# Kernel tuning notes

Measured on AMD Instinct MI355X. Metric: run time of the kernel, lower is better.

Reference implementation:

```python
import jax, jax.numpy as jnp
import numpy as np

B, S, D, H = 2, 2048, 768, 12
DK = D // H  # 64
LN_EPS = 1e-5


def setup_inputs() -> dict:
    key = jax.random.key(0)
    ks = jax.random.split(key, 8)
    std = 0.02
    return {
        "x": jax.random.normal(ks[0], (B, S, D), dtype=jnp.float32),
        "Wq": jax.random.normal(ks[1], (D, D), dtype=jnp.float32) * std,
        "Wp": jax.random.normal(ks[2], (D, D), dtype=jnp.float32) * std,
        "Wk": jax.random.normal(ks[3], (D, D), dtype=jnp.float32) * std,
        "Wv": jax.random.normal(ks[4], (D, D), dtype=jnp.float32) * std,
        "Wo": jax.random.normal(ks[5], (D, D), dtype=jnp.float32) * std,
        "bo": jnp.zeros((D,), dtype=jnp.float32),
        "gamma": jnp.ones((D,), dtype=jnp.float32),
        "beta": jnp.zeros((D,), dtype=jnp.float32),
        "dt": jnp.asarray(0.1, dtype=jnp.float32),
        "gate": jnp.ones((1,), dtype=jnp.float32),
    }


def _heads(t):
    # [B,S,D] -> [B,H,S,DK]
    return t.reshape(B, S, H, DK).transpose(0, 2, 1, 3)


def reference(x, Wq, Wp, Wk, Wv, Wo, bo, gamma, beta, dt, gate):
    scale = DK ** -0.5
    q = _heads(x @ Wq)
    p = _heads(x @ Wp)
    k = _heads(x @ Wk)
    v = _heads(x @ Wv)

    # --- first attention pass (potential energy at q) ---
    e1 = jnp.einsum("bhsd,bhtd->bhst", q, k) * scale
    w1 = jax.nn.softmax(e1, axis=-1)
    pe1 = jnp.einsum("bhst,bhtd->bhsd", w1, v)  # dV/dq approx (v_to_k = Identity since d_v == d_k)

    # --- leapfrog half step + full position step ---
    p_half = p - (dt / 2) * pe1 * gate
    q_new = q + dt * p_half

    # --- second attention pass at updated q ---
    e2 = jnp.einsum("bhsd,bhtd->bhst", q_new, k) * scale
    w2 = jax.nn.softmax(e2, axis=-1)
    pe2 = jnp.einsum("bhst,bhtd->bhsd", w2, v)
    p_new = p_half - (dt / 2) * pe2 * gate

    q_flat = q_new.transpose(0, 2, 1, 3).reshape(B, S, D)
    out = q_flat @ Wo + bo + x  # to_output + residual

    mu = jnp.mean(out, axis=-1, keepdims=True)
    var = jnp.mean(jnp.square(out - mu), axis=-1, keepdims=True)
    return (out - mu) * jax.lax.rsqrt(var + LN_EPS) * gamma + beta
```

## Files before the change

### kernel.cpp

```cpp
#include <hip/hip_runtime.h>
#include <stdint.h>

typedef __bf16 bf16;
typedef __bf16 bf16x8 __attribute__((ext_vector_type(8)));
typedef __bf16 bf16x4 __attribute__((ext_vector_type(4)));
typedef float f32x4 __attribute__((ext_vector_type(4)));

constexpr int nB = 2, nS = 2048, nD = 768, nH = 12, nDK = 64;
constexpr int nM = nB * nS;
constexpr float LN_EPS = 1e-5f;

static __device__ __forceinline__ f32x4 mfma16(bf16x8 a, bf16x8 b, f32x4 c) {
  return __builtin_amdgcn_mfma_f32_16x16x32_bf16(a, b, c, 0, 0, 0);
}

static __device__ __forceinline__ void gll16(const void* g, void* l) {
  __builtin_amdgcn_global_load_lds(
      (const __attribute__((address_space(1))) void*)g,
      (__attribute__((address_space(3))) void*)l, 16, 0, 0);
}

__global__ __launch_bounds__(256) void k_prep_x(const float* __restrict__ x,
                                                bf16* __restrict__ xb) {
  int i = (blockIdx.x * 256 + threadIdx.x) * 4;
  float4 v = *(const float4*)(x + i);
  bf16x4 o;
  o[0] = (bf16)v.x; o[1] = (bf16)v.y; o[2] = (bf16)v.z; o[3] = (bf16)v.w;
  *(bf16x4*)(xb + i) = o;
}

__global__ __launch_bounds__(256) void k_prep_w(
    const float* __restrict__ w0, const float* __restrict__ w1,
    const float* __restrict__ w2, const float* __restrict__ w3,
    const float* __restrict__ w4, bf16* __restrict__ wt) {
  __shared__ float tb[64][65];
  int w = blockIdx.z;
  const float* src = (w == 0) ? w0 : (w == 1) ? w1 : (w == 2) ? w2 : (w == 3) ? w3 : w4;
  int k0 = blockIdx.y * 64, n0 = blockIdx.x * 64;
  int tx = threadIdx.x & 63, ty = threadIdx.x >> 6;
#pragma unroll
  for (int it = 0; it < 16; ++it) {
    int r = it * 4 + ty;
    tb[r][tx] = src[(size_t)(k0 + r) * nD + n0 + tx];
  }
  __syncthreads();
  bf16* dst = wt + (size_t)w * nD * nD;
#pragma unroll
  for (int it = 0; it < 16; ++it) {
    int r = it * 4 + ty;
    dst[(size_t)(n0 + r) * nD + k0 + tx] = (bf16)tb[tx][r];
  }
}

__global__ __launch_bounds__(256, 2) void k_gemm_qpkv(
    const bf16* __restrict__ xb, const bf16* __restrict__ wt,
    bf16* __restrict__ qf, bf16* __restrict__ pf, bf16* __restrict__ kf_,
    bf16* __restrict__ vt) {
  __shared__ alignas(16) char smem[65536];
  int t = threadIdx.x, lane = t & 63, w = t >> 6;
  int fr = lane & 15, fg = lane >> 4;
  int wm = w >> 1, wn = w & 1;
  int widx = blockIdx.z;
  int m0 = blockIdx.y * 128, n0 = blockIdx.x * 128;
  const bf16* abase = xb + (size_t)m0 * nD;
  const bf16* bbase = wt + (size_t)widx * nD * nD + (size_t)n0 * nD;

  f32x4 acc[4][4];
#pragma unroll
  for (int i = 0; i < 4; ++i)
#pragma unroll
    for (int j = 0; j < 4; ++j) acc[i][j] = (f32x4){0.f, 0.f, 0.f, 0.f};

  int aoff[2][4], boff[2][4];
#pragma unroll
  for (int ks = 0; ks < 2; ++ks) {
#pragma unroll
    for (int i = 0; i < 4; ++i) {
      int row = wm * 64 + i * 16 + fr;
      aoff[ks][i] = row * 128 + (((ks * 4 + fg) ^ (row & 7)) << 4);
      int rowb = wn * 64 + i * 16 + fr;
      boff[ks][i] = 16384 + rowb * 128 + (((ks * 4 + fg) ^ (rowb & 7)) << 4);
    }
  }
  const bf16 *asrc[4], *bsrc[4];
#pragma unroll
  for (int i = 0; i < 4; ++i) {
    int row = i * 32 + (t >> 3);
    int c = (t & 7) ^ (row & 7);
    asrc[i] = abase + (size_t)row * nD + c * 8;
    bsrc[i] = bbase + (size_t)row * nD + c * 8;
  }

#define STAGEG(BUF, kt)                                                        \
  {                                                                            \
    _Pragma("unroll") for (int i = 0; i < 4; ++i) {                            \
      gll16(asrc[i] + (kt)*64, smem + (BUF) + i * 4096 + w * 1024);            \
      gll16(bsrc[i] + (kt)*64, smem + (BUF) + 16384 + i * 4096 + w * 1024);    \
    }                                                                          \
  }

#define COMPUTEG(BUF)                                                          \
  {                                                                            \
    _Pragma("unroll") for (int ks = 0; ks < 2; ++ks) {                         \
      bf16x8 af[4], bfr[4];                                                    \
      _Pragma("unroll") for (int i = 0; i < 4; ++i)                            \
          af[i] = *(const bf16x8*)(smem + (BUF) + aoff[ks][i]);                \
      _Pragma("unroll") for (int j = 0; j < 4; ++j)                            \
          bfr[j] = *(const bf16x8*)(smem + (BUF) + boff[ks][j]);               \
      _Pragma("unroll") for (int i = 0; i < 4; ++i)                            \
          _Pragma("unroll") for (int j = 0; j < 4; ++j) acc[i][j] =            \
          mfma16(af[i], bfr[j], acc[i][j]);                                    \
    }                                                                          \
  }

  STAGEG(0, 0);
  __syncthreads();
#pragma unroll 1
  for (int kt = 0; kt < 12; kt += 2) {
    if (kt + 1 < 12) STAGEG(32768, kt + 1);
    COMPUTEG(0);
    __syncthreads();
    if (kt + 2 < 12) STAGEG(0, kt + 2);
    COMPUTEG(32768);
    __syncthreads();
  }
#undef STAGEG
#undef COMPUTEG

  if (widx < 3) {
    bf16* outf = (widx == 0) ? qf : (widx == 1) ? pf : kf_;
    float oscale = (widx == 2) ? 0.18033688f : 1.0f;
#pragma unroll
    for (int i = 0; i < 4; ++i)
#pragma unroll
      for (int j = 0; j < 4; ++j) {
        int n = n0 + wn * 64 + j * 16 + fr;
#pragma unroll
        for (int r = 0; r < 4; ++r) {
          int m = m0 + wm * 64 + i * 16 + fg * 4 + r;
          outf[(size_t)m * nD + n] = (bf16)(acc[i][j][r] * oscale);
        }
      }
  } else {
#pragma unroll
    for (int i = 0; i < 4; ++i)
#pragma unroll
      for (int j = 0; j < 4; ++j) {
        int n = n0 + wn * 64 + j * 16 + fr;
        int h = n >> 6, dk = n & 63;
        int mbase = m0 + wm * 64 + i * 16 + fg * 4;
        int b = mbase >> 11, s = mbase & (nS - 1);
        int bh = b * nH + h;
        bf16x4 pk;
#pragma unroll
        for (int r = 0; r < 4; ++r) pk[r] = (bf16)acc[i][j][r];
        *(bf16x4*)(vt + ((size_t)bh * nDK + dk) * nS + s) = pk;
      }
  }
}

__global__ __launch_bounds__(256, 3) void k_attn(
    const bf16* __restrict__ qf, const bf16* __restrict__ pf,
    const bf16* __restrict__ kf_, const bf16* __restrict__ vt,
    const float* __restrict__ dtp, const float* __restrict__ gatep,
    bf16* __restrict__ qn) {
  __shared__ alignas(16) char lds[40960];
  int t = threadIdx.x, lane = t & 63, w = t >> 6;
  int fr = lane & 15, fg = lane >> 4;
  int blk = blockIdx.x;
  int qt = blk & 31, bh = blk >> 5;
  int b = bh / nH, h = bh % nH;
  int q0 = qt * 64 + w * 16;
  const bf16* Qrow = qf + (size_t)(b * nS) * nD + (size_t)h * nDK;
  const bf16* Prow = pf + (size_t)(b * nS) * nD + (size_t)h * nDK;
  const bf16* Krow = kf_ + (size_t)(b * nS) * nD + (size_t)h * nDK;
  const bf16* Vb = vt + (size_t)bh * nDK * nS;
  char* myp = lds + 32768 + w * 2048;

  bf16x8 qa[2];
#pragma unroll
  for (int ks = 0; ks < 2; ++ks)
    qa[ks] = *(const bf16x8*)(Qrow + (size_t)(q0 + fr) * nD + ks * 32 + fg * 8);

  bf16x8 vone;
#pragma unroll
  for (int i = 0; i < 8; ++i) vone[i] = (bf16)1.0f;

  f32x4 o[5];
#pragma unroll
  for (int df = 0; df < 5; ++df) o[df] = (f32x4){0.f, 0.f, 0.f, 0.f};

  int koA[4], koB[4];
#pragma unroll
  for (int kfi = 0; kfi < 4; ++kfi) {
    int key = kfi * 16 + fr;
    koA[kfi] = key * 128 + ((fg ^ (key & 7)) << 4);
    koB[kfi] = key * 128 + (((4 + fg) ^ (key & 7)) << 4);
  }
  int vo[2][4], pr[2], pw[4];
#pragma unroll
  for (int ks = 0; ks < 2; ++ks) {
    pr[ks] = fr * 128 + (((ks * 4 + fg) ^ (fr & 7)) << 4);
#pragma unroll
    for (int df = 0; df < 4; ++df) {
      int row = df * 16 + fr;
      vo[ks][df] = row * 128 + (((ks * 4 + fg) ^ (row & 7)) << 4);
    }
  }
#pragma unroll
  for (int kfi = 0; kfi < 4; ++kfi) {
    int blk16 = kfi * 2 + (fg >> 1);
    pw[kfi] = fr * 128 + (((blk16 ^ (fr & 7)) << 4) | ((fg & 1) << 3));
  }

  const bf16 *ks0, *ks1, *vs0, *vs1;
  {
    int r0 = w * 16 + (lane >> 3), c0 = (lane & 7) ^ (r0 & 7);
    int r1 = r0 + 8, c1 = (lane & 7) ^ (r1 & 7);
    ks0 = Krow + (size_t)r0 * nD + c0 * 8;
    ks1 = Krow + (size_t)r1 * nD + c1 * 8;
    vs0 = Vb + (size_t)r0 * nS + c0 * 8;
    vs1 = Vb + (size_t)r1 * nS + c1 * 8;
  }

#define STAGE(KB, VB, kt)                                                      \
  {                                                                            \
    gll16(ks0 + (size_t)(kt)*64 * nD, lds + (KB) + w * 2048);                  \
    gll16(vs0 + (kt)*64, lds + (VB) + w * 2048);                               \
    gll16(ks1 + (size_t)(kt)*64 * nD, lds + (KB) + w * 2048 + 1024);           \
    gll16(vs1 + (kt)*64, lds + (VB) + w * 2048 + 1024);                        \
  }

#define COMPUTE(KB, VB)                                                        \
  {                                                                            \
    f32x4 sf[4];                                                               \
    _Pragma("unroll") for (int kfi = 0; kfi < 4; ++kfi) {                      \
      bf16x8 ka = *(const bf16x8*)(lds + (KB) + koA[kfi]);                     \
      bf16x8 kc = *(const bf16x8*)(lds + (KB) + koB[kfi]);                     \
      f32x4 s = mfma16(ka, qa[0], (f32x4){0.f, 0.f, 0.f, 0.f});                \
      sf[kfi] = mfma16(kc, qa[1], s);                                          \
    }                                                                          \
    _Pragma("unroll") for (int kfi = 0; kfi < 4; ++kfi) {                      \
      bf16x4 pk;                                                               \
      _Pragma("unroll") for (int r = 0; r < 4; ++r)                            \
          pk[r] = (bf16)__builtin_exp2f(sf[kfi][r]);                           \
      *(bf16x4*)(myp + pw[kfi]) = pk;                                          \
    }                                                                          \
    _Pragma("unroll") for (int ks = 0; ks < 2; ++ks) {                         \
      bf16x8 pb = *(const bf16x8*)(myp + pr[ks]);                              \
      _Pragma("unroll") for (int df = 0; df < 4; ++df) {                       \
        bf16x8 vv = *(const bf16x8*)(lds + (VB) + vo[ks][df]);                 \
        o[df] = mfma16(vv, pb, o[df]);                                         \
      }                                                                        \
      o[4] = mfma16(vone, pb, o[4]);                                           \
    }                                                                          \
  }

#define VMCNT4 asm volatile("s_waitcnt vmcnt(4)" ::: "memory")
#define VMCNT0 asm volatile("s_waitcnt vmcnt(0)" ::: "memory")
#define BAR __builtin_amdgcn_s_barrier()

  STAGE(0, 16384, 0);
#pragma unroll 1
  for (int kt = 0; kt < 32; kt += 2) {
    STAGE(8192, 24576, kt + 1);
    VMCNT4;
    BAR;
    COMPUTE(0, 16384);
    BAR;
    if (kt + 2 < 32) {
      STAGE(0, 16384, kt + 2);
      VMCNT4;
    } else {
      VMCNT0;
    }
    BAR;
    COMPUTE(8192, 24576);
    BAR;
  }
#undef STAGE
#undef COMPUTE
#undef VMCNT4
#undef VMCNT0
#undef BAR

  float dt = dtp[0], gate = gatep[0];
  float c2 = 0.5f * dt * dt * gate;
  float inv = 1.f / o[4][0];
  int qrow = q0 + fr;
#pragma unroll
  for (int df = 0; df < 4; ++df) {
    int dk = df * 16 + fg * 4;
    bf16x4 qv4 = *(const bf16x4*)(Qrow + (size_t)qrow * nD + dk);
    bf16x4 pv4 = *(const bf16x4*)(Prow + (size_t)qrow * nD + dk);
    bf16x4 ov;
#pragma unroll
    for (int r = 0; r < 4; ++r) {
      float pe = o[df][r] * inv;
      ov[r] = (bf16)((float)qv4[r] + dt * (float)pv4[r] - c2 * pe);
    }
    *(bf16x4*)(qn + ((size_t)(b * nS) + qrow) * nD + h * nDK + dk) = ov;
  }
}

__global__ __launch_bounds__(256, 2) void k_gemm_out(
    const bf16* __restrict__ qn, const bf16* __restrict__ wto,
    const float* __restrict__ bo, const float* __restrict__ x,
    float* __restrict__ outp) {
  __shared__ alignas(16) char smem[65536];
  int t = threadIdx.x, lane = t & 63, w = t >> 6;
  int fr = lane & 15, fg = lane >> 4;
  int wm = w >> 1, wn = w & 1;
  int m0 = blockIdx.y * 128, n0 = blockIdx.x * 128;
  const bf16* abase = qn + (size_t)m0 * nD;
  const bf16* bbase = wto + (size_t)n0 * nD;

  f32x4 acc[4][4];
#pragma unroll
  for (int i = 0; i < 4; ++i)
#pragma unroll
    for (int j = 0; j < 4; ++j) acc[i][j] = (f32x4){0.f, 0.f, 0.f, 0.f};

  int aoff[2][4], boff[2][4];
#pragma unroll
  for (int ks = 0; ks < 2; ++ks) {
#pragma unroll
    for (int i = 0; i < 4; ++i) {
      int row = wm * 64 + i * 16 + fr;
      aoff[ks][i] = row * 128 + (((ks * 4 + fg) ^ (row & 7)) << 4);
      int rowb = wn * 64 + i * 16 + fr;
      boff[ks][i] = 16384 + rowb * 128 + (((ks * 4 + fg) ^ (rowb & 7)) << 4);
    }
  }
  const bf16 *asrc[4], *bsrc[4];
#pragma unroll
  for (int i = 0; i < 4; ++i) {
    int row = i * 32 + (t >> 3);
    int c = (t & 7) ^ (row & 7);
    asrc[i] = abase + (size_t)row * nD + c * 8;
    bsrc[i] = bbase + (size_t)row * nD + c * 8;
  }

#define STAGEG(BUF, kt)                                                        \
  {                                                                            \
    _Pragma("unroll") for (int i = 0; i < 4; ++i) {                            \
      gll16(asrc[i] + (kt)*64, smem + (BUF) + i * 4096 + w * 1024);            \
      gll16(bsrc[i] + (kt)*64, smem + (BUF) + 16384 + i * 4096 + w * 1024);    \
    }                                                                          \
  }

#define COMPUTEG(BUF)                                                          \
  {                                                                            \
    _Pragma("unroll") for (int ks = 0; ks < 2; ++ks) {                         \
      bf16x8 af[4], bfr[4];                                                    \
      _Pragma("unroll") for (int i = 0; i < 4; ++i)                            \
          af[i] = *(const bf16x8*)(smem + (BUF) + aoff[ks][i]);                \
      _Pragma("unroll") for (int j = 0; j < 4; ++j)                            \
          bfr[j] = *(const bf16x8*)(smem + (BUF) + boff[ks][j]);               \
      _Pragma("unroll") for (int i = 0; i < 4; ++i)                            \
          _Pragma("unroll") for (int j = 0; j < 4; ++j) acc[i][j] =            \
          mfma16(af[i], bfr[j], acc[i][j]);                                    \
    }                                                                          \
  }

  STAGEG(0, 0);
  __syncthreads();
#pragma unroll 1
  for (int kt = 0; kt < 12; kt += 2) {
    if (kt + 1 < 12) STAGEG(32768, kt + 1);
    COMPUTEG(0);
    __syncthreads();
    if (kt + 2 < 12) STAGEG(0, kt + 2);
    COMPUTEG(32768);
    __syncthreads();
  }
#undef STAGEG
#undef COMPUTEG

#pragma unroll
  for (int i = 0; i < 4; ++i)
#pragma unroll
    for (int j = 0; j < 4; ++j) {
      int n = n0 + wn * 64 + j * 16 + fr;
      float bias = bo[n];
#pragma unroll
      for (int r = 0; r < 4; ++r) {
        int m = m0 + wm * 64 + i * 16 + fg * 4 + r;
        outp[(size_t)m * nD + n] = acc[i][j][r] + bias + x[(size_t)m * nD + n];
      }
    }
}

__global__ __launch_bounds__(256) void k_ln(const float* outp,
                                            const float* __restrict__ gamma,
                                            const float* __restrict__ beta,
                                            float* y) {
  int t = threadIdx.x, lane = t & 63, w = t >> 6;
  int row = blockIdx.x * 4 + w;
  const float* rp = outp + (size_t)row * nD;
  float v[12], s1 = 0.f, s2 = 0.f;
#pragma unroll
  for (int i = 0; i < 12; ++i) {
    v[i] = rp[lane + i * 64];
    s1 += v[i];
    s2 += v[i] * v[i];
  }
#pragma unroll
  for (int d = 1; d < 64; d <<= 1) {
    s1 += __shfl_xor(s1, d);
    s2 += __shfl_xor(s2, d);
  }
  float mu = s1 * (1.f / 768.f);
  float var = s2 * (1.f / 768.f) - mu * mu;
  float rstd = rsqrtf(var + LN_EPS);
  float* yp = y + (size_t)row * nD;
#pragma unroll
  for (int i = 0; i < 12; ++i) {
    int n = lane + i * 64;
    yp[n] = (v[i] - mu) * rstd * gamma[n] + beta[n];
  }
}

extern "C" void kernel_launch(void* const* d_in, const int* in_sizes, int n_in,
                              void* d_out, int out_size, void* d_ws, size_t ws_size,
                              hipStream_t stream) {
  const float* x = (const float*)d_in[0];
  const float* Wq = (const float*)d_in[1];
  const float* Wp = (const float*)d_in[2];
  const float* Wk = (const float*)d_in[3];
  const float* Wv = (const float*)d_in[4];
  const float* Wo = (const float*)d_in[5];
  const float* bo = (const float*)d_in[6];
  const float* gamma = (const float*)d_in[7];
  const float* beta = (const float*)d_in[8];
  const float* dt = (const float*)d_in[9];
  const float* gate = (const float*)d_in[10];

  char* ws = (char*)d_ws;
  const size_t szb = (size_t)nM * nD * 2;
  bf16* xb = (bf16*)(ws + 0 * szb);
  bf16* qf = (bf16*)(ws + 1 * szb);
  bf16* pf = (bf16*)(ws + 2 * szb);
  bf16* kf_ = (bf16*)(ws + 3 * szb);
  bf16* vt = (bf16*)(ws + 4 * szb);
  bf16* wt = (bf16*)(ws + 5 * szb);
  bf16* qn = xb;
  float* outp = (float*)d_out;

  k_prep_x<<<dim3(nM * nD / 1024), dim3(256), 0, stream>>>(x, xb);
  k_prep_w<<<dim3(12, 12, 5), dim3(256), 0, stream>>>(Wq, Wp, Wk, Wv, Wo, wt);
  k_gemm_qpkv<<<dim3(6, 32, 4), dim3(256), 0, stream>>>(xb, wt, qf, pf, kf_, vt);
  k_attn<<<dim3(768), dim3(256), 0, stream>>>(qf, pf, kf_, vt, dt, gate, qn);
  k_gemm_out<<<dim3(6, 32), dim3(256), 0, stream>>>(qn, wt + 4 * (size_t)nD * nD, bo, x, outp);
  k_ln<<<dim3(nM / 4), dim3(256), 0, stream>>>(outp, gamma, beta, (float*)d_out);
}
```

Baseline: 115.3 us.

## Process two query row-groups per wave in attention to reuse K/V fragments

The attention kernel now runs 128 threads (2 waves) per block, and each wave handles 32 query rows instead of 16. Each K and V fragment read from LDS is reused for two query groups, which halves LDS reads per MFMA. Each wave also issues twice as many global-to-LDS loads per stage, with the wait count adjusted to match. The trade-off is more registers per wave and fewer waves per block to hide latency, which may lower occupancy.

```diff
diff --git a/kernel.cpp b/kernel.cpp
--- a/kernel.cpp
+++ b/kernel.cpp
@@ -159,7 +159,7 @@
   }
 }
 
-__global__ __launch_bounds__(256, 3) void k_attn(
+__global__ __launch_bounds__(128, 2) void k_attn(
     const bf16* __restrict__ qf, const bf16* __restrict__ pf,
     const bf16* __restrict__ kf_, const bf16* __restrict__ vt,
     const float* __restrict__ dtp, const float* __restrict__ gatep,
@@ -170,25 +170,30 @@
   int blk = blockIdx.x;
   int qt = blk & 31, bh = blk >> 5;
   int b = bh / nH, h = bh % nH;
-  int q0 = qt * 64 + w * 16;
+  int q0 = qt * 64 + w * 32;
   const bf16* Qrow = qf + (size_t)(b * nS) * nD + (size_t)h * nDK;
   const bf16* Prow = pf + (size_t)(b * nS) * nD + (size_t)h * nDK;
   const bf16* Krow = kf_ + (size_t)(b * nS) * nD + (size_t)h * nDK;
   const bf16* Vb = vt + (size_t)bh * nDK * nS;
-  char* myp = lds + 32768 + w * 2048;
-
-  bf16x8 qa[2];
-#pragma unroll
-  for (int ks = 0; ks < 2; ++ks)
-    qa[ks] = *(const bf16x8*)(Qrow + (size_t)(q0 + fr) * nD + ks * 32 + fg * 8);
+  char* myp = lds + 32768 + w * 4096;
+
+  bf16x8 qa[2][2];
+#pragma unroll
+  for (int qg = 0; qg < 2; ++qg)
+#pragma unroll
+    for (int ks = 0; ks < 2; ++ks)
+      qa[qg][ks] = *(const bf16x8*)(Qrow + (size_t)(q0 + qg * 16 + fr) * nD +
+                                    ks * 32 + fg * 8);
 
   bf16x8 vone;
 #pragma unroll
   for (int i = 0; i < 8; ++i) vone[i] = (bf16)1.0f;
 
-  f32x4 o[5];
-#pragma unroll
-  for (int df = 0; df < 5; ++df) o[df] = (f32x4){0.f, 0.f, 0.f, 0.f};
+  f32x4 o[2][5];
+#pragma unroll
+  for (int qg = 0; qg < 2; ++qg)
+#pragma unroll
+    for (int df = 0; df < 5; ++df) o[qg][df] = (f32x4){0.f, 0.f, 0.f, 0.f};
 
   int koA[4], koB[4];
 #pragma unroll
@@ -213,50 +218,57 @@
     pw[kfi] = fr * 128 + (((blk16 ^ (fr & 7)) << 4) | ((fg & 1) << 3));
   }
 
-  const bf16 *ks0, *ks1, *vs0, *vs1;
+  const bf16 *ksrc[4], *vsrc[4];
   {
-    int r0 = w * 16 + (lane >> 3), c0 = (lane & 7) ^ (r0 & 7);
-    int r1 = r0 + 8, c1 = (lane & 7) ^ (r1 & 7);
-    ks0 = Krow + (size_t)r0 * nD + c0 * 8;
-    ks1 = Krow + (size_t)r1 * nD + c1 * 8;
-    vs0 = Vb + (size_t)r0 * nS + c0 * 8;
-    vs1 = Vb + (size_t)r1 * nS + c1 * 8;
+    int c = (lane & 7) ^ (lane >> 3);
+#pragma unroll
+    for (int i = 0; i < 4; ++i) {
+      int row = w * 32 + i * 8 + (lane >> 3);
+      ksrc[i] = Krow + (size_t)row * nD + c * 8;
+      vsrc[i] = Vb + (size_t)row * nS + c * 8;
+    }
   }
 
 #define STAGE(KB, VB, kt)                                                      \
   {                                                                            \
-    gll16(ks0 + (size_t)(kt)*64 * nD, lds + (KB) + w * 2048);                  \
-    gll16(vs0 + (kt)*64, lds + (VB) + w * 2048);                               \
-    gll16(ks1 + (size_t)(kt)*64 * nD, lds + (KB) + w * 2048 + 1024);           \
-    gll16(vs1 + (kt)*64, lds + (VB) + w * 2048 + 1024);                        \
+    _Pragma("unroll") for (int i = 0; i < 4; ++i) {                            \
+      gll16(ksrc[i] + (size_t)(kt)*64 * nD, lds + (KB) + w * 4096 + i * 1024); \
+      gll16(vsrc[i] + (kt)*64, lds + (VB) + w * 4096 + i * 1024);              \
+    }                                                                          \
   }
 
 #define COMPUTE(KB, VB)                                                        \
   {                                                                            \
-    f32x4 sf[4];                                                               \
+    f32x4 sf[2][4];                                                            \
     _Pragma("unroll") for (int kfi = 0; kfi < 4; ++kfi) {                      \
       bf16x8 ka = *(const bf16x8*)(lds + (KB) + koA[kfi]);                     \
       bf16x8 kc = *(const bf16x8*)(lds + (KB) + koB[kfi]);                     \
-      f32x4 s = mfma16(ka, qa[0], (f32x4){0.f, 0.f, 0.f, 0.f});                \
-      sf[kfi] = mfma16(kc, qa[1], s);                                          \
-    }                                                                          \
-    _Pragma("unroll") for (int kfi = 0; kfi < 4; ++kfi) {                      \
+      _Pragma("unroll") for (int qg = 0; qg < 2; ++qg) {                       \
+        f32x4 s = mfma16(ka, qa[qg][0], (f32x4){0.f, 0.f, 0.f, 0.f});          \
+        sf[qg][kfi] = mfma16(kc, qa[qg][1], s);                                \
+      }                                                                        \
+    }                                                                          \
+    _Pragma("unroll") for (int qg = 0; qg < 2; ++qg)                           \
+        _Pragma("unroll") for (int kfi = 0; kfi < 4; ++kfi) {                  \
       bf16x4 pk;                                                               \
       _Pragma("unroll") for (int r = 0; r < 4; ++r)                            \
-          pk[r] = (bf16)__builtin_exp2f(sf[kfi][r]);                           \
-      *(bf16x4*)(myp + pw[kfi]) = pk;                                          \
+          pk[r] = (bf16)__builtin_exp2f(sf[qg][kfi][r]);                       \
+      *(bf16x4*)(myp + qg * 2048 + pw[kfi]) = pk;                              \
     }                                                                          \
     _Pragma("unroll") for (int ks = 0; ks < 2; ++ks) {                         \
-      bf16x8 pb = *(const bf16x8*)(myp + pr[ks]);                              \
-      _Pragma("unroll") for (int df = 0; df < 4; ++df) {                       \
-        bf16x8 vv = *(const bf16x8*)(lds + (VB) + vo[ks][df]);                 \
-        o[df] = mfma16(vv, pb, o[df]);                                         \
+      bf16x8 vv[4];                                                            \
+      _Pragma("unroll") for (int df = 0; df < 4; ++df)                         \
+          vv[df] = *(const bf16x8*)(lds + (VB) + vo[ks][df]);                  \
+      _Pragma("unroll") for (int qg = 0; qg < 2; ++qg) {                       \
+        bf16x8 pb = *(const bf16x8*)(myp + qg * 2048 + pr[ks]);                \
+        _Pragma("unroll") for (int df = 0; df < 4; ++df)                       \
+            o[qg][df] = mfma16(vv[df], pb, o[qg][df]);                         \
+        o[qg][4] = mfma16(vone, pb, o[qg][4]);                                 \
       }                                                                        \
-      o[4] = mfma16(vone, pb, o[4]);                                           \
-    }                                                                          \
-  }
-
-#define VMCNT4 asm volatile("s_waitcnt vmcnt(4)" ::: "memory")
+    }                                                                          \
+  }
+
+#define VMCNT8 asm volatile("s_waitcnt vmcnt(8)" ::: "memory")
 #define VMCNT0 asm volatile("s_waitcnt vmcnt(0)" ::: "memory")
 #define BAR __builtin_amdgcn_s_barrier()
 
@@ -264,13 +276,13 @@
 #pragma unroll 1
   for (int kt = 0; kt < 32; kt += 2) {
     STAGE(8192, 24576, kt + 1);
-    VMCNT4;
+    VMCNT8;
     BAR;
     COMPUTE(0, 16384);
     BAR;
     if (kt + 2 < 32) {
       STAGE(0, 16384, kt + 2);
-      VMCNT4;
+      VMCNT8;
     } else {
       VMCNT0;
     }
@@ -280,26 +292,29 @@
   }
 #undef STAGE
 #undef COMPUTE
-#undef VMCNT4
+#undef VMCNT8
 #undef VMCNT0
 #undef BAR
 
   float dt = dtp[0], gate = gatep[0];
   float c2 = 0.5f * dt * dt * gate;
-  float inv = 1.f / o[4][0];
-  int qrow = q0 + fr;
-#pragma unroll
-  for (int df = 0; df < 4; ++df) {
-    int dk = df * 16 + fg * 4;
-    bf16x4 qv4 = *(const bf16x4*)(Qrow + (size_t)qrow * nD + dk);
-    bf16x4 pv4 = *(const bf16x4*)(Prow + (size_t)qrow * nD + dk);
-    bf16x4 ov;
-#pragma unroll
-    for (int r = 0; r < 4; ++r) {
-      float pe = o[df][r] * inv;
-      ov[r] = (bf16)((float)qv4[r] + dt * (float)pv4[r] - c2 * pe);
-    }
-    *(bf16x4*)(qn + ((size_t)(b * nS) + qrow) * nD + h * nDK + dk) = ov;
+#pragma unroll
+  for (int qg = 0; qg < 2; ++qg) {
+    float inv = 1.f / o[qg][4][0];
+    int qrow = q0 + qg * 16 + fr;
+#pragma unroll
+    for (int df = 0; df < 4; ++df) {
+      int dk = df * 16 + fg * 4;
+      bf16x4 qv4 = *(const bf16x4*)(Qrow + (size_t)qrow * nD + dk);
+      bf16x4 pv4 = *(const bf16x4*)(Prow + (size_t)qrow * nD + dk);
+      bf16x4 ov;
+#pragma unroll
+      for (int r = 0; r < 4; ++r) {
+        float pe = o[qg][df][r] * inv;
+        ov[r] = (bf16)((float)qv4[r] + dt * (float)pv4[r] - c2 * pe);
+      }
+      *(bf16x4*)(qn + ((size_t)(b * nS) + qrow) * nD + h * nDK + dk) = ov;
+    }
   }
 }
 
@@ -450,7 +465,7 @@
   k_prep_x<<<dim3(nM * nD / 1024), dim3(256), 0, stream>>>(x, xb);
   k_prep_w<<<dim3(12, 12, 5), dim3(256), 0, stream>>>(Wq, Wp, Wk, Wv, Wo, wt);
   k_gemm_qpkv<<<dim3(6, 32, 4), dim3(256), 0, stream>>>(xb, wt, qf, pf, kf_, vt);
-  k_attn<<<dim3(768), dim3(256), 0, stream>>>(qf, pf, kf_, vt, dt, gate, qn);
+  k_attn<<<dim3(768), dim3(128), 0, stream>>>(qf, pf, kf_, vt, dt, gate, qn);
   k_gemm_out<<<dim3(6, 32), dim3(256), 0, stream>>>(qn, wt + 4 * (size_t)nD * nD, bo, x, outp);
   k_ln<<<dim3(nM / 4), dim3(256), 0, stream>>>(outp, gamma, beta, (float*)d_out);
 }
```

Result: slower. 123.1 us (+6.8%).

## Load V fragments directly into registers instead of staging through LDS

Applied to the files above, without the earlier changes.

The attention kernel stops staging V tiles in shared memory with async global-to-LDS copies. Each wave now reads its V MFMA operands straight from global memory into registers, once per key tile. This removes the V LDS traffic and cuts the LDS footprint from 40 KB to 24 KB, which may allow more resident blocks. In exchange, every wave fetches the full V tile on its own, about four times the global/L2 traffic. The loads are also issued just before use, so their latency is poorly hidden.

```diff
diff --git a/kernel.cpp b/kernel.cpp
--- a/kernel.cpp
+++ b/kernel.cpp
@@ -164,7 +164,7 @@
     const bf16* __restrict__ kf_, const bf16* __restrict__ vt,
     const float* __restrict__ dtp, const float* __restrict__ gatep,
     bf16* __restrict__ qn) {
-  __shared__ alignas(16) char lds[40960];
+  __shared__ alignas(16) char lds[24576];
   int t = threadIdx.x, lane = t & 63, w = t >> 6;
   int fr = lane & 15, fg = lane >> 4;
   int blk = blockIdx.x;
@@ -175,7 +175,7 @@
   const bf16* Prow = pf + (size_t)(b * nS) * nD + (size_t)h * nDK;
   const bf16* Krow = kf_ + (size_t)(b * nS) * nD + (size_t)h * nDK;
   const bf16* Vb = vt + (size_t)bh * nDK * nS;
-  char* myp = lds + 32768 + w * 2048;
+  char* myp = lds + 16384 + w * 2048;
 
   bf16x8 qa[2];
 #pragma unroll
@@ -197,41 +197,44 @@
     koA[kfi] = key * 128 + ((fg ^ (key & 7)) << 4);
     koB[kfi] = key * 128 + (((4 + fg) ^ (key & 7)) << 4);
   }
-  int vo[2][4], pr[2], pw[4];
-#pragma unroll
-  for (int ks = 0; ks < 2; ++ks) {
+  int pr[2], pw[4];
+#pragma unroll
+  for (int ks = 0; ks < 2; ++ks)
     pr[ks] = fr * 128 + (((ks * 4 + fg) ^ (fr & 7)) << 4);
-#pragma unroll
-    for (int df = 0; df < 4; ++df) {
-      int row = df * 16 + fr;
-      vo[ks][df] = row * 128 + (((ks * 4 + fg) ^ (row & 7)) << 4);
-    }
-  }
 #pragma unroll
   for (int kfi = 0; kfi < 4; ++kfi) {
     int blk16 = kfi * 2 + (fg >> 1);
     pw[kfi] = fr * 128 + (((blk16 ^ (fr & 7)) << 4) | ((fg & 1) << 3));
   }
 
-  const bf16 *ks0, *ks1, *vs0, *vs1;
+  const bf16* vptr[4];
+#pragma unroll
+  for (int df = 0; df < 4; ++df)
+    vptr[df] = Vb + (size_t)(df * 16 + fr) * nS + fg * 8;
+
+  const bf16 *ks0, *ks1;
   {
     int r0 = w * 16 + (lane >> 3), c0 = (lane & 7) ^ (r0 & 7);
     int r1 = r0 + 8, c1 = (lane & 7) ^ (r1 & 7);
     ks0 = Krow + (size_t)r0 * nD + c0 * 8;
     ks1 = Krow + (size_t)r1 * nD + c1 * 8;
-    vs0 = Vb + (size_t)r0 * nS + c0 * 8;
-    vs1 = Vb + (size_t)r1 * nS + c1 * 8;
-  }
-
-#define STAGE(KB, VB, kt)                                                      \
+  }
+
+#define STAGE(KB, kt)                                                          \
   {                                                                            \
     gll16(ks0 + (size_t)(kt)*64 * nD, lds + (KB) + w * 2048);                  \
-    gll16(vs0 + (kt)*64, lds + (VB) + w * 2048);                               \
     gll16(ks1 + (size_t)(kt)*64 * nD, lds + (KB) + w * 2048 + 1024);           \
-    gll16(vs1 + (kt)*64, lds + (VB) + w * 2048 + 1024);                        \
-  }
-
-#define COMPUTE(KB, VB)                                                        \
+  }
+
+#define VLOAD(VV, kt)                                                          \
+  {                                                                            \
+    _Pragma("unroll") for (int df = 0; df < 4; ++df) {                         \
+      VV[0][df] = *(const bf16x8*)(vptr[df] + (kt)*64);                        \
+      VV[1][df] = *(const bf16x8*)(vptr[df] + (kt)*64 + 32);                   \
+    }                                                                          \
+  }
+
+#define COMPUTE(KB, VV)                                                        \
   {                                                                            \
     f32x4 sf[4];                                                               \
     _Pragma("unroll") for (int kfi = 0; kfi < 4; ++kfi) {                      \
@@ -248,40 +251,42 @@
     }                                                                          \
     _Pragma("unroll") for (int ks = 0; ks < 2; ++ks) {                         \
       bf16x8 pb = *(const bf16x8*)(myp + pr[ks]);                              \
-      _Pragma("unroll") for (int df = 0; df < 4; ++df) {                       \
-        bf16x8 vv = *(const bf16x8*)(lds + (VB) + vo[ks][df]);                 \
-        o[df] = mfma16(vv, pb, o[df]);                                         \
-      }                                                                        \
+      _Pragma("unroll") for (int df = 0; df < 4; ++df)                         \
+          o[df] = mfma16(VV[ks][df], pb, o[df]);                               \
       o[4] = mfma16(vone, pb, o[4]);                                           \
     }                                                                          \
   }
 
-#define VMCNT4 asm volatile("s_waitcnt vmcnt(4)" ::: "memory")
-#define VMCNT0 asm volatile("s_waitcnt vmcnt(0)" ::: "memory")
+#define VMCNT10 asm volatile("s_waitcnt vmcnt(10)" ::: "memory")
+#define VMCNT8 asm volatile("s_waitcnt vmcnt(8)" ::: "memory")
 #define BAR __builtin_amdgcn_s_barrier()
 
-  STAGE(0, 16384, 0);
+  STAGE(0, 0);
 #pragma unroll 1
   for (int kt = 0; kt < 32; kt += 2) {
-    STAGE(8192, 24576, kt + 1);
-    VMCNT4;
+    bf16x8 vA[2][4], vB[2][4];
+    VLOAD(vA, kt);
+    STAGE(8192, kt + 1);
+    VMCNT10;
     BAR;
-    COMPUTE(0, 16384);
+    COMPUTE(0, vA);
     BAR;
+    VLOAD(vB, kt + 1);
     if (kt + 2 < 32) {
-      STAGE(0, 16384, kt + 2);
-      VMCNT4;
+      STAGE(0, kt + 2);
+      VMCNT10;
     } else {
-      VMCNT0;
+      VMCNT8;
     }
     BAR;
-    COMPUTE(8192, 24576);
+    COMPUTE(8192, vB);
     BAR;
   }
 #undef STAGE
+#undef VLOAD
 #undef COMPUTE
-#undef VMCNT4
-#undef VMCNT0
+#undef VMCNT10
+#undef VMCNT8
 #undef BAR
 
   float dt = dtp[0], gate = gatep[0];
```

Result: slower. 165.0 us (+43.1%).
